# Performance work log

Measured on AMD Instinct MI355X. Metric: run time of the kernel, lower is better.

The kernel has to match this reference:

```python
import jax, jax.numpy as jnp
import numpy as np

H_DIM = 64; GRID = 8; G = GRID * GRID; NEIGH = 2.0
ATT = 1024; EMB = 4
S = 32; P = 64; B = S * P


def setup_inputs() -> dict:
    key = jax.random.key(0)
    ks = jax.random.split(key, 20)
    bounds = jnp.arange(0, B + 1, P, dtype=jnp.int32)
    seq_start_end = jnp.stack([bounds[:-1], bounds[1:]], axis=1)  # (S,2) uniform scenes
    def lin(k, fan_in, shape):
        return jax.random.normal(k, shape, jnp.float32) / np.sqrt(fan_in)
    return {
        "h_states": jax.random.normal(ks[0], (1, B, H_DIM), jnp.float32),
        "seq_start_end": seq_start_end,
        "end_pos": jax.random.uniform(ks[1], (B, 2), jnp.float32) * 4.0,
        "rel_pos": jax.random.normal(ks[2], (B, 2), jnp.float32),
        # Attention_Decoder params
        "W_enc": lin(ks[3], H_DIM, (H_DIM, ATT)), "b_enc": jnp.zeros((ATT,), jnp.float32),
        "W_dec": lin(ks[4], H_DIM, (H_DIM, ATT)), "b_dec": jnp.zeros((ATT,), jnp.float32),
        "w_full": lin(ks[5], ATT, (ATT,)), "b_full": jnp.zeros((), jnp.float32),
        "W_embed": lin(ks[6], 4, (4, EMB)), "b_embed": jnp.zeros((EMB,), jnp.float32),
        "W_out": lin(ks[7], H_DIM + EMB, (H_DIM + EMB, ATT)), "b_out": jnp.zeros((ATT,), jnp.float32),
        # mlp_pool params (Linear -> BatchNorm -> ReLU)
        "W_mlp": lin(ks[8], ATT, (ATT, ATT)), "b_mlp": jnp.zeros((ATT,), jnp.float32),
        "bn_gamma": jnp.ones((ATT,), jnp.float32), "bn_beta": jnp.zeros((ATT,), jnp.float32),
    }


def social_pool(h, end_pos):
    # h: (B, H), end_pos: (B, 2); uniform scenes S x P
    pos = end_pos.reshape(S, P, 2)
    hid = h.reshape(S, P, H_DIM)
    ax = pos[:, :, None, 0]; ay = pos[:, :, None, 1]  # anchor (S,P,1)
    ox = pos[:, None, :, 0]; oy = pos[:, None, :, 1]  # other  (S,1,P)
    half = NEIGH / 2
    tl_x = ax - half; tl_y = ay + half
    br_x = ax + half; br_y = ay - half
    cell_x = jnp.floor((ox - tl_x) / NEIGH * GRID)
    cell_y = jnp.floor((tl_y - oy) / NEIGH * GRID)
    grid = (cell_x + cell_y * GRID).astype(jnp.int32)  # (S,P,P)
    oob = (ox >= br_x) | (ox <= tl_x) | (oy >= tl_y) | (oy <= br_y)
    oob = oob | jnp.eye(P, dtype=bool)[None]  # self-pairs excluded (within_bound[0::P+1]=1)
    anchor_off = (jnp.arange(P, dtype=jnp.int32) * G)[None, :, None]
    idx = jnp.where(oob, 0, grid + 1 + anchor_off)  # slot 0 = dump slot
    seq_off = (jnp.arange(S, dtype=jnp.int32) * (P * G + 1))[:, None, None]
    flat_idx = (idx + seq_off).reshape(-1)
    vals = jnp.broadcast_to(hid[:, None, :, :], (S, P, P, H_DIM)).reshape(-1, H_DIM)
    buf = jnp.zeros((S * (P * G + 1), H_DIM), h.dtype).at[flat_idx].add(vals)
    buf = buf.reshape(S, P * G + 1, H_DIM)[:, 1:, :]  # drop dump slot per scene
    return buf.reshape(B, G, H_DIM)


def reference(h_states, seq_start_end, end_pos, rel_pos,
              W_enc, b_enc, W_dec, b_dec, w_full, b_full,
              W_embed, b_embed, W_out, b_out, W_mlp, b_mlp, bn_gamma, bn_beta):
    del seq_start_end  # uniform scene layout baked into S, P
    h = h_states.reshape(-1, H_DIM)                      # (B, H)
    enc = social_pool(h, end_pos)                        # (B, G, H)
    dec_a = h @ W_dec + b_dec                            # (B, ATT)
    enc_a = jnp.einsum('bgh,ha->bga', enc, W_enc) + b_enc
    scores = jax.nn.relu(enc_a + dec_a[:, None, :]) @ w_full + b_full  # (B, G)
    alpha = jax.nn.softmax(scores, axis=-1)
    ctx = jnp.einsum('bg,bgh->bh', alpha, enc)           # (B, H)
    embed_info = jnp.concatenate([end_pos, rel_pos], axis=1)  # (B, 4)
    emb = jax.nn.relu(embed_info @ W_embed + b_embed)
    out = jax.nn.relu(jnp.concatenate([ctx, emb], axis=1) @ W_out + b_out)  # (B, ATT)
    # mlp_pool: Linear -> BatchNorm1d (training-mode batch stats) -> ReLU
    x = out @ W_mlp + b_mlp
    mu = jnp.mean(x, axis=0)
    var = jnp.var(x, axis=0)
    x = (x - mu) * jax.lax.rsqrt(var + 1e-5) * bn_gamma + bn_beta
    return jax.nn.relu(x)
```

## Files before the change

kernel.cpp:

```cpp
#include <hip/hip_runtime.h>
#include <hip/hip_bf16.h>
#include <math.h>

#define H_DIM 64
#define G 64
#define ATT 1024
#define EMB 4
#define P 64
#define BB 2048
#define MAXROWS 129088
#define PREP_BLOCKS 817
#define MAGICF 0x13579BDF

typedef __attribute__((ext_vector_type(8))) short short8;
typedef __attribute__((ext_vector_type(4))) float floatx4;

__device__ inline ushort f2bf(float v) {
    __hip_bfloat16 b = __float2bfloat16(v);
    return *(ushort*)&b;
}
__device__ inline float bf2f(ushort u) {
    union { float f; unsigned u32; } x;
    x.u32 = ((unsigned)u) << 16;
    return x.f;
}

__global__ __launch_bounds__(256) void prep_kernel(const float* __restrict__ h,
                                                   const float* __restrict__ end_pos,
                                                   const float* __restrict__ W_enc,
                                                   const float* __restrict__ W_dec,
                                                   const float* __restrict__ W_out,
                                                   const float* __restrict__ W_mlp,
                                                   ushort* __restrict__ enc,
                                                   ushort* __restrict__ h_bf,
                                                   ushort* __restrict__ Wte,
                                                   ushort* __restrict__ Wdt,
                                                   ushort* __restrict__ Wot,
                                                   ushort* __restrict__ Wt,
                                                   int* __restrict__ rowidx,
                                                   int* __restrict__ cntA,
                                                   int* __restrict__ baseA,
                                                   int* __restrict__ counter,
                                                   float* __restrict__ sums,
                                                   int* __restrict__ flag) {
    __shared__ float tileT[64][65];
    __shared__ int nzS[4], baseSh[4];

    int blk = blockIdx.x;
    int t = threadIdx.x;

    if (blk == 0) {
        if (t < 64) __hip_atomic_store(&counter[t], 0, __ATOMIC_RELAXED, __HIP_MEMORY_SCOPE_AGENT);
        int* sz = (int*)sums;
        for (int i = t; i < 2048; i += 256)
            __hip_atomic_store(&sz[i], 0, __ATOMIC_RELAXED, __HIP_MEMORY_SCOPE_AGENT);
        __syncthreads();
        if (t == 0) __hip_atomic_store(flag, MAGICF, __ATOMIC_RELEASE, __HIP_MEMORY_SCOPE_AGENT);
    } else if (blk <= 512) {
        int wv = t >> 6, lane = t & 63;
        int b = (blk - 1) * 4 + wv;
        int s = b >> 6, i = b & 63;
        const float* pseq = end_pos + (size_t)s * P * 2;
        const float* hrow = h + (size_t)s * P * H_DIM;

        float2 pj = ((const float2*)pseq)[lane];
        float ax = __shfl(pj.x, i), ay = __shfl(pj.y, i);
        float tlx = ax - 1.f, tly = ay + 1.f, brx = ax + 1.f, bry = ay - 1.f;
        bool oob = (pj.x >= brx) || (pj.x <= tlx) || (pj.y >= tly) || (pj.y <= bry) || (lane == i);
        int cx = (int)floorf((pj.x - tlx) * 4.0f);
        int cy = (int)floorf((tly - pj.y) * 4.0f);
        int g = cx + cy * 8;

        unsigned long long hitmask = __ballot(!oob);
        unsigned long long m = hitmask, cellmask = 0ull;
        while (m) {
            int j = __builtin_ctzll(m); m &= m - 1;
            int gj = __shfl(g, j);
            cellmask |= 1ull << gj;
        }
        int n_nz = __popcll(cellmask);
        if (lane == 0) nzS[wv] = n_nz;

        h_bf[(size_t)b * 64 + lane] = f2bf(h[(size_t)b * 64 + lane]);

        __syncthreads();
        if (t == 0) {
            while (__hip_atomic_load(flag, __ATOMIC_ACQUIRE, __HIP_MEMORY_SCOPE_AGENT) != MAGICF) {}
            int n0 = nzS[0], n1 = nzS[1], n2 = nzS[2], n3 = nzS[3];
            int base = atomicAdd(counter, n0 + n1 + n2 + n3);
            baseSh[0] = base;
            baseSh[1] = base + n0;
            baseSh[2] = base + n0 + n1;
            baseSh[3] = base + n0 + n1 + n2;
        }
        __syncthreads();
        int base = baseSh[wv];
        if (lane == 0) { cntA[b] = n_nz; baseA[b] = base; }

        unsigned long long cm = cellmask;
        int slot = 0;
        while (cm) {
            int gg = __builtin_ctzll(cm); cm &= cm - 1;
            unsigned long long jm = __ballot((!oob) && (g == gg));
            float sum = 0.f;
            while (jm) {
                int j = __builtin_ctzll(jm); jm &= jm - 1;
                sum += hrow[j * H_DIM + lane];
            }
            enc[((size_t)(b * G + gg)) * H_DIM + lane] = f2bf(sum);
            if (lane == 0) rowidx[base + slot] = b * G + gg;
            ++slot;
        }
    } else if (blk <= 528) {
        int n0 = (blk - 513) * 64;
        #pragma unroll
        for (int idx = 0; idx < 16; ++idx) {
            int flat = t + 256 * idx;
            int k = flat >> 6, c = flat & 63;
            tileT[k][c] = W_enc[(size_t)k * ATT + n0 + c];
        }
        __syncthreads();
        #pragma unroll
        for (int idx = 0; idx < 16; ++idx) {
            int flat = t + 256 * idx;
            int n = flat >> 6, k = flat & 63;
            Wte[(size_t)(n0 + n) * 64 + k] = f2bf(tileT[k][n]);
        }
    } else if (blk <= 544) {
        int n0 = (blk - 529) * 64;
        #pragma unroll
        for (int idx = 0; idx < 16; ++idx) {
            int flat = t + 256 * idx;
            int k = flat >> 6, c = flat & 63;
            tileT[k][c] = W_dec[(size_t)k * ATT + n0 + c];
        }
        __syncthreads();
        #pragma unroll
        for (int idx = 0; idx < 16; ++idx) {
            int flat = t + 256 * idx;
            int n = flat >> 6, k = flat & 63;
            Wdt[(size_t)(n0 + n) * 64 + k] = f2bf(tileT[k][n]);
        }
    } else if (blk <= 560) {
        int n0 = (blk - 545) * 64;
        int n = t & 63, kg = t >> 6;
        #pragma unroll
        for (int kk = 0; kk < 24; ++kk) {
            int k = kg * 24 + kk;
            float v = (k < 68) ? W_out[(size_t)k * ATT + n0 + n] : 0.f;
            Wot[(size_t)(n0 + n) * 96 + k] = f2bf(v);
        }
    } else {
        int idx2 = blk - 561;
        int k0 = (idx2 & 15) * 64, n0 = (idx2 >> 4) * 64;
        #pragma unroll
        for (int idx = 0; idx < 16; ++idx) {
            int flat = t + 256 * idx;
            int r = flat >> 6, c = flat & 63;
            tileT[r][c] = W_mlp[(size_t)(k0 + r) * ATT + n0 + c];
        }
        __syncthreads();
        #pragma unroll
        for (int idx = 0; idx < 16; ++idx) {
            int flat = t + 256 * idx;
            int r = flat >> 6, c = flat & 63;
            Wt[(size_t)(n0 + r) * ATT + k0 + c] = f2bf(tileT[c][r]);
        }
    }
}

__global__ __launch_bounds__(256) void dec_mfma_kernel(const ushort* __restrict__ A,
                                                       const ushort* __restrict__ Bt,
                                                       const float* __restrict__ b_dec,
                                                       const float* __restrict__ b_enc,
                                                       const float* __restrict__ w_full,
                                                       float* __restrict__ dec_r,
                                                       float* __restrict__ s_part) {
    int t = threadIdx.x;
    int w = t >> 6, lane = t & 63;
    int lm = lane & 15, q = lane >> 4;
    int m0 = blockIdx.x * 64, n1 = blockIdx.y * 128;
    __shared__ __align__(16) ushort Asm[64][72];
    __shared__ __align__(16) ushort Bsm[128][72];

    #pragma unroll
    for (int i = 0; i < 4; ++i) {
        int flat = t + 256 * i;
        int r = flat >> 4, c4 = (flat & 15) * 4;
        *(uint2*)&Asm[r][c4] = *(const uint2*)&A[(size_t)(m0 + r) * 64 + c4];
    }
    #pragma unroll
    for (int i = 0; i < 8; ++i) {
        int flat = t + 256 * i;
        int r = flat >> 4, c4 = (flat & 15) * 4;
        *(uint2*)&Bsm[r][c4] = *(const uint2*)&Bt[(size_t)(n1 + r) * 64 + c4];
    }
    __syncthreads();

    floatx4 acc[4][2];
    #pragma unroll
    for (int mt = 0; mt < 4; ++mt)
        #pragma unroll
        for (int nt = 0; nt < 2; ++nt) acc[mt][nt] = (floatx4){0.f, 0.f, 0.f, 0.f};

    #pragma unroll
    for (int ks = 0; ks < 64; ks += 32) {
        short8 af[4], bfr[2];
        #pragma unroll
        for (int mt = 0; mt < 4; ++mt)
            af[mt] = *(const short8*)&Asm[mt * 16 + lm][ks + q * 8];
        #pragma unroll
        for (int nt = 0; nt < 2; ++nt)
            bfr[nt] = *(const short8*)&Bsm[w * 32 + nt * 16 + lm][ks + q * 8];
        #pragma unroll
        for (int mt = 0; mt < 4; ++mt)
            #pragma unroll
            for (int nt = 0; nt < 2; ++nt)
                acc[mt][nt] = __builtin_amdgcn_mfma_f32_16x16x32_bf16(af[mt], bfr[nt], acc[mt][nt], 0, 0, 0);
    }

    float part[4][4];
    #pragma unroll
    for (int mt = 0; mt < 4; ++mt)
        #pragma unroll
        for (int r = 0; r < 4; ++r) part[mt][r] = 0.f;

    #pragma unroll
    for (int nt = 0; nt < 2; ++nt) {
        int col = n1 + w * 32 + nt * 16 + lm;
        float bcol = b_dec[col] + b_enc[col];
        float wf = w_full[col];
        #pragma unroll
        for (int mt = 0; mt < 4; ++mt)
            #pragma unroll
            for (int r = 0; r < 4; ++r) {
                int row = m0 + mt * 16 + q * 4 + r;
                float v = acc[mt][nt][r] + bcol;
                dec_r[(size_t)row * ATT + col] = v;
                part[mt][r] += fmaxf(v, 0.f) * wf;
            }
    }
    #pragma unroll
    for (int mt = 0; mt < 4; ++mt)
        #pragma unroll
        for (int r = 0; r < 4; ++r) {
            float v = part[mt][r];
            v += __shfl_xor(v, 1); v += __shfl_xor(v, 2);
            v += __shfl_xor(v, 4); v += __shfl_xor(v, 8);
            part[mt][r] = v;
        }
    if (lm == 0) {
        int sp = blockIdx.y * 4 + w;
        #pragma unroll
        for (int mt = 0; mt < 4; ++mt)
            #pragma unroll
            for (int r = 0; r < 4; ++r)
                s_part[(size_t)sp * 2048 + m0 + mt * 16 + q * 4 + r] = part[mt][r];
    }
}

__global__ __launch_bounds__(256) void scoresC_mfma_kernel(const ushort* __restrict__ enc,
                                                           const int* __restrict__ rowidx,
                                                           const int* __restrict__ counter,
                                                           const float* __restrict__ dec_r,
                                                           const ushort* __restrict__ Wte,
                                                           const float* __restrict__ w_full,
                                                           const float* __restrict__ b_full,
                                                           float* __restrict__ score_c) {
    int M = counter[0];
    int row0 = blockIdx.x * 64;
    if (row0 >= M) return;
    int t = threadIdx.x;
    int w = t >> 6, lane = t & 63;
    int lm = lane & 15, q = lane >> 4;

    __shared__ __align__(16) ushort AS[64][72];
    __shared__ __align__(16) ushort BS[256][72];
    __shared__ int rowS[64];
    __shared__ float redS[4][64];

    if (t < 64) rowS[t] = (row0 + t < M) ? rowidx[row0 + t] : 0;
    __syncthreads();
    #pragma unroll
    for (int i = 0; i < 4; ++i) {
        int flat = t + 256 * i;
        int r = flat >> 4, c4 = (flat & 15) * 4;
        *(uint2*)&AS[r][c4] = *(const uint2*)&enc[(size_t)rowS[r] * 64 + c4];
    }
    int bbr[16];
    #pragma unroll
    for (int mt = 0; mt < 4; ++mt)
        #pragma unroll
        for (int r = 0; r < 4; ++r)
            bbr[mt * 4 + r] = rowS[mt * 16 + q * 4 + r] >> 6;

    float part[4][4];
    #pragma unroll
    for (int mt = 0; mt < 4; ++mt)
        #pragma unroll
        for (int r = 0; r < 4; ++r) part[mt][r] = 0.f;

    for (int c = 0; c < 4; ++c) {
        __syncthreads();
        #pragma unroll
        for (int i = 0; i < 16; ++i) {
            int flat = t + 256 * i;
            int r = flat >> 4, c4 = (flat & 15) * 4;
            *(uint2*)&BS[r][c4] = *(const uint2*)&Wte[(size_t)(c * 256 + r) * 64 + c4];
        }
        __syncthreads();

        floatx4 acc[4][4];
        #pragma unroll
        for (int mt = 0; mt < 4; ++mt)
            #pragma unroll
            for (int nt = 0; nt < 4; ++nt) acc[mt][nt] = (floatx4){0.f, 0.f, 0.f, 0.f};

        #pragma unroll
        for (int ks = 0; ks < 64; ks += 32) {
            short8 af[4], bfr[4];
            #pragma unroll
            for (int mt = 0; mt < 4; ++mt)
                af[mt] = *(const short8*)&AS[mt * 16 + lm][ks + q * 8];
            #pragma unroll
            for (int nt = 0; nt < 4; ++nt)
                bfr[nt] = *(const short8*)&BS[w * 64 + nt * 16 + lm][ks + q * 8];
            #pragma unroll
            for (int mt = 0; mt < 4; ++mt)
                #pragma unroll
                for (int nt = 0; nt < 4; ++nt)
                    acc[mt][nt] = __builtin_amdgcn_mfma_f32_16x16x32_bf16(af[mt], bfr[nt], acc[mt][nt], 0, 0, 0);
        }

        int colbase = c * 256 + w * 64;
        #pragma unroll
        for (int nt = 0; nt < 4; ++nt) {
            int col = colbase + nt * 16 + lm;
            float wf = w_full[col];
            #pragma unroll
            for (int mt = 0; mt < 4; ++mt)
                #pragma unroll
                for (int r = 0; r < 4; ++r) {
                    float v = acc[mt][nt][r] + dec_r[(size_t)bbr[mt * 4 + r] * ATT + col];
                    part[mt][r] += fmaxf(v, 0.f) * wf;
                }
        }
    }
    #pragma unroll
    for (int mt = 0; mt < 4; ++mt)
        #pragma unroll
        for (int r = 0; r < 4; ++r) {
            float v = part[mt][r];
            v += __shfl_xor(v, 1); v += __shfl_xor(v, 2);
            v += __shfl_xor(v, 4); v += __shfl_xor(v, 8);
            part[mt][r] = v;
        }
    if (lm == 0) {
        #pragma unroll
        for (int mt = 0; mt < 4; ++mt)
            #pragma unroll
            for (int r = 0; r < 4; ++r)
                redS[w][mt * 16 + q * 4 + r] = part[mt][r];
    }
    __syncthreads();
    if (t < 64) {
        int row = row0 + t;
        if (row < M)
            score_c[row] = redS[0][t] + redS[1][t] + redS[2][t] + redS[3][t] + b_full[0];
    }
}

__global__ __launch_bounds__(64) void softmax_ctx_kernel(const float* __restrict__ score_c,
                                                         const int* __restrict__ rowidx,
                                                         const int* __restrict__ cntA,
                                                         const int* __restrict__ baseA,
                                                         const float* __restrict__ s_part,
                                                         const ushort* __restrict__ enc,
                                                         const float* __restrict__ end_pos,
                                                         const float* __restrict__ rel_pos,
                                                         const float* __restrict__ W_embed,
                                                         const float* __restrict__ b_embed,
                                                         const float* __restrict__ b_full,
                                                         ushort* __restrict__ ctx_bf) {
    int b = blockIdx.x, t = threadIdx.x;
    int cnt = cntA[b], base = baseA[b];
    float sp = (t < 32) ? s_part[(size_t)t * 2048 + b] : 0.f;
    #pragma unroll
    for (int o = 32; o > 0; o >>= 1) sp += __shfl_xor(sp, o);
    float se = sp + b_full[0];
    float sc = se;
    int ri = 0;
    if (t < cnt) { sc = score_c[base + t]; ri = rowidx[base + t]; }
    float mx = sc;
    #pragma unroll
    for (int o = 32; o > 0; o >>= 1) mx = fmaxf(mx, __shfl_xor(mx, o));
    float e = expf(sc - mx);
    float ssum = e;
    #pragma unroll
    for (int o = 32; o > 0; o >>= 1) ssum += __shfl_xor(ssum, o);
    __shared__ float aS[G];
    __shared__ int rS[G];
    aS[t] = e / ssum;
    rS[t] = ri;
    __syncthreads();
    float ctx = 0.f;
    for (int i = 0; i < cnt; ++i)
        ctx += aS[i] * bf2f(enc[(size_t)rS[i] * H_DIM + t]);
    ctx_bf[(size_t)b * 96 + t] = f2bf(ctx);
    if (t < EMB) {
        float e0 = end_pos[2*b], e1 = end_pos[2*b+1], e2 = rel_pos[2*b], e3 = rel_pos[2*b+1];
        float v = b_embed[t] + e0 * W_embed[0*EMB + t] + e1 * W_embed[1*EMB + t]
                             + e2 * W_embed[2*EMB + t] + e3 * W_embed[3*EMB + t];
        ctx_bf[(size_t)b * 96 + 64 + t] = f2bf(v > 0.f ? v : 0.f);
    }
    if (t < 28) ctx_bf[(size_t)b * 96 + 68 + t] = 0;
}

__global__ __launch_bounds__(256) void out_mfma_kernel(const ushort* __restrict__ A,
                                                       const ushort* __restrict__ Bt,
                                                       const float* __restrict__ bias,
                                                       ushort* __restrict__ out) {
    int t = threadIdx.x;
    int w = t >> 6, lane = t & 63;
    int lm = lane & 15, q = lane >> 4;
    int m0 = blockIdx.x * 64, n1 = blockIdx.y * 128;
    __shared__ __align__(16) ushort Asm[64][104];
    __shared__ __align__(16) ushort Bsm[128][104];

    {
        int r = t >> 2, pp = t & 3;
        #pragma unroll
        for (int ii = 0; ii < 3; ++ii) {
            int c8 = (pp * 3 + ii) * 8;
            *(uint4*)&Asm[r][c8] = *(const uint4*)&A[(size_t)(m0 + r) * 96 + c8];
        }
    }
    {
        int r = t >> 1, pp = t & 1;
        #pragma unroll
        for (int ii = 0; ii < 6; ++ii) {
            int c8 = (pp * 6 + ii) * 8;
            *(uint4*)&Bsm[r][c8] = *(const uint4*)&Bt[(size_t)(n1 + r) * 96 + c8];
        }
    }
    __syncthreads();

    floatx4 acc[4][2];
    #pragma unroll
    for (int mt = 0; mt < 4; ++mt)
        #pragma unroll
        for (int nt = 0; nt < 2; ++nt) acc[mt][nt] = (floatx4){0.f, 0.f, 0.f, 0.f};

    #pragma unroll
    for (int ks = 0; ks < 96; ks += 32) {
        short8 af[4], bfr[2];
        #pragma unroll
        for (int mt = 0; mt < 4; ++mt)
            af[mt] = *(const short8*)&Asm[mt * 16 + lm][ks + q * 8];
        #pragma unroll
        for (int nt = 0; nt < 2; ++nt)
            bfr[nt] = *(const short8*)&Bsm[w * 32 + nt * 16 + lm][ks + q * 8];
        #pragma unroll
        for (int mt = 0; mt < 4; ++mt)
            #pragma unroll
            for (int nt = 0; nt < 2; ++nt)
                acc[mt][nt] = __builtin_amdgcn_mfma_f32_16x16x32_bf16(af[mt], bfr[nt], acc[mt][nt], 0, 0, 0);
    }
    #pragma unroll
    for (int nt = 0; nt < 2; ++nt) {
        int col = n1 + w * 32 + nt * 16 + lm;
        float bv = bias[col];
        #pragma unroll
        for (int mt = 0; mt < 4; ++mt)
            #pragma unroll
            for (int r = 0; r < 4; ++r) {
                int row = m0 + mt * 16 + q * 4 + r;
                out[(size_t)row * ATT + col] = f2bf(fmaxf(acc[mt][nt][r] + bv, 0.f));
            }
    }
}

__global__ __launch_bounds__(256) void mlp_mfma_kernel(const ushort* __restrict__ A,
                                                       const ushort* __restrict__ Bt,
                                                       const float* __restrict__ bias,
                                                       float* __restrict__ X,
                                                       float* __restrict__ sums) {
    int t = threadIdx.x;
    int w = t >> 6, lane = t & 63;
    int lm = lane & 15, q = lane >> 4;
    int m0 = blockIdx.x * 64, n0 = blockIdx.y * 64;
    __shared__ __align__(16) ushort Asm[64][72];
    __shared__ __align__(16) ushort Bsm[64][72];

    floatx4 acc[4];
    #pragma unroll
    for (int mt = 0; mt < 4; ++mt) acc[mt] = (floatx4){0.f, 0.f, 0.f, 0.f};

    for (int k0 = 0; k0 < 1024; k0 += 64) {
        __syncthreads();
        #pragma unroll
        for (int i = 0; i < 4; ++i) {
            int flat = t + 256 * i;
            int r = flat >> 4, c4 = (flat & 15) * 4;
            *(uint2*)&Asm[r][c4] = *(const uint2*)&A[(size_t)(m0 + r) * 1024 + k0 + c4];
            *(uint2*)&Bsm[r][c4] = *(const uint2*)&Bt[(size_t)(n0 + r) * 1024 + k0 + c4];
        }
        __syncthreads();
        #pragma unroll
        for (int ks = 0; ks < 64; ks += 32) {
            short8 af[4], bfr;
            #pragma unroll
            for (int mt = 0; mt < 4; ++mt)
                af[mt] = *(const short8*)&Asm[mt * 16 + lm][ks + q * 8];
            bfr = *(const short8*)&Bsm[w * 16 + lm][ks + q * 8];
            #pragma unroll
            for (int mt = 0; mt < 4; ++mt)
                acc[mt] = __builtin_amdgcn_mfma_f32_16x16x32_bf16(af[mt], bfr, acc[mt], 0, 0, 0);
        }
    }
    int col = n0 + w * 16 + lm;
    float bv = bias[col];
    float s1 = 0.f, s2 = 0.f;
    #pragma unroll
    for (int mt = 0; mt < 4; ++mt)
        #pragma unroll
        for (int r = 0; r < 4; ++r) {
            int row = m0 + mt * 16 + q * 4 + r;
            float v = acc[mt][r] + bv;
            X[(size_t)row * 1024 + col] = v;
            s1 += v; s2 += v * v;
        }
    s1 += __shfl_xor(s1, 16); s1 += __shfl_xor(s1, 32);
    s2 += __shfl_xor(s2, 16); s2 += __shfl_xor(s2, 32);
    if (q == 0) {
        atomicAdd(&sums[col], s1);
        atomicAdd(&sums[ATT + col], s2);
    }
}

__global__ __launch_bounds__(256) void bn_kernel(const float* __restrict__ X,
                                                 const float* __restrict__ sums,
                                                 const float* __restrict__ gamma,
                                                 const float* __restrict__ beta,
                                                 float* __restrict__ out) {
    size_t i4 = ((size_t)blockIdx.x * 256 + threadIdx.x) * 4;
    int f = (int)(i4 & 1023);
    float4 xv = *(const float4*)&X[i4];
    float4 s1 = *(const float4*)&sums[f];
    float4 s2 = *(const float4*)&sums[ATT + f];
    float4 gm = *(const float4*)&gamma[f];
    float4 bt = *(const float4*)&beta[f];
    float4 ov;
    float mu, var, v;
    mu = s1.x * (1.f / BB); var = s2.x * (1.f / BB) - mu * mu;
    v = (xv.x - mu) * rsqrtf(var + 1e-5f) * gm.x + bt.x; ov.x = v > 0.f ? v : 0.f;
    mu = s1.y * (1.f / BB); var = s2.y * (1.f / BB) - mu * mu;
    v = (xv.y - mu) * rsqrtf(var + 1e-5f) * gm.y + bt.y; ov.y = v > 0.f ? v : 0.f;
    mu = s1.z * (1.f / BB); var = s2.z * (1.f / BB) - mu * mu;
    v = (xv.z - mu) * rsqrtf(var + 1e-5f) * gm.z + bt.z; ov.z = v > 0.f ? v : 0.f;
    mu = s1.w * (1.f / BB); var = s2.w * (1.f / BB) - mu * mu;
    v = (xv.w - mu) * rsqrtf(var + 1e-5f) * gm.w + bt.w; ov.w = v > 0.f ? v : 0.f;
    *(float4*)&out[i4] = ov;
}

extern "C" void kernel_launch(void* const* d_in, const int* in_sizes, int n_in,
                              void* d_out, int out_size, void* d_ws, size_t ws_size,
                              hipStream_t stream) {
    const float* h        = (const float*)d_in[0];
    const float* end_pos  = (const float*)d_in[2];
    const float* rel_pos  = (const float*)d_in[3];
    const float* W_enc    = (const float*)d_in[4];
    const float* b_enc    = (const float*)d_in[5];
    const float* W_dec    = (const float*)d_in[6];
    const float* b_dec    = (const float*)d_in[7];
    const float* w_full   = (const float*)d_in[8];
    const float* b_full   = (const float*)d_in[9];
    const float* W_embed  = (const float*)d_in[10];
    const float* b_embed  = (const float*)d_in[11];
    const float* W_out    = (const float*)d_in[12];
    const float* b_out    = (const float*)d_in[13];
    const float* W_mlp    = (const float*)d_in[14];
    const float* b_mlp    = (const float*)d_in[15];
    const float* bn_gamma = (const float*)d_in[16];
    const float* bn_beta  = (const float*)d_in[17];

    float* ws = (float*)d_ws;
    ushort* enc     = (ushort*)ws;
    ushort* h_bf    = (ushort*)(ws + 4194304);
    ushort* Wte     = (ushort*)(ws + 4259840);
    ushort* Wdt     = (ushort*)(ws + 4292608);
    ushort* Wot     = (ushort*)(ws + 4325376);
    ushort* Wt      = (ushort*)(ws + 4374528);
    ushort* ctx_bf  = (ushort*)(ws + 4898816);
    ushort* out_bf  = (ushort*)(ws + 4997120);
    float*  x       = ws + 6045696;
    float*  dec_r   = ws + 8388608;
    int*    rowidx  = (int*)(ws + 10485760);
    float*  score_c = ws + 10616832;
    int*    cntA    = (int*)(ws + 10747904);
    int*    baseA   = (int*)(ws + 10749952);
    int*    counter = (int*)(ws + 10752000);
    float*  sums    = ws + 10752064;
    float*  s_part  = ws + 10754112;
    int*    flag    = (int*)(ws + 10819648);

    prep_kernel<<<PREP_BLOCKS, 256, 0, stream>>>(h, end_pos, W_enc, W_dec, W_out, W_mlp,
                                                 enc, h_bf, Wte, Wdt, Wot, Wt,
                                                 rowidx, cntA, baseA, counter, sums, flag);
    dec_mfma_kernel<<<dim3(32, 8), 256, 0, stream>>>(h_bf, Wdt, b_dec, b_enc, w_full, dec_r, s_part);
    scoresC_mfma_kernel<<<MAXROWS / 64, 256, 0, stream>>>(enc, rowidx, counter, dec_r, Wte,
                                                          w_full, b_full, score_c);
    softmax_ctx_kernel<<<BB, 64, 0, stream>>>(score_c, rowidx, cntA, baseA, s_part, enc,
                                              end_pos, rel_pos, W_embed, b_embed, b_full, ctx_bf);
    out_mfma_kernel<<<dim3(32, 8), 256, 0, stream>>>(ctx_bf, Wot, b_out, out_bf);
    mlp_mfma_kernel<<<dim3(32, 16), 256, 0, stream>>>(out_bf, Wt, b_mlp, x, sums);
    bn_kernel<<<2048, 256, 0, stream>>>(x, sums, bn_gamma, bn_beta, (float*)d_out);
}
```

Before: 167.2 us.

## Fuse decoder GEMM into prep kernel, converting h and W_dec on the fly

The decoder projection GEMM (h @ W_dec plus bias, relu dot with w_full) now runs as extra blocks inside the prep kernel. Those blocks read fp32 h and W_dec directly and convert them to bf16 in shared memory. This removes one kernel launch and the intermediate h_bf and Wdt buffers, along with their global round-trip. The cost is a larger shared-memory footprint per prep block, which may reduce occupancy for the other block roles, and uncoalesced transposing loads of W_dec.

```diff
diff --git a/kernel.cpp b/kernel.cpp
--- a/kernel.cpp
+++ b/kernel.cpp
@@ -9,7 +9,7 @@
 #define P 64
 #define BB 2048
 #define MAXROWS 129088
-#define PREP_BLOCKS 817
+#define K1_BLOCKS 1057
 #define MAGICF 0x13579BDF
 
 typedef __attribute__((ext_vector_type(8))) short short8;
@@ -31,19 +31,22 @@
                                                    const float* __restrict__ W_dec,
                                                    const float* __restrict__ W_out,
                                                    const float* __restrict__ W_mlp,
+                                                   const float* __restrict__ b_dec,
+                                                   const float* __restrict__ b_enc,
+                                                   const float* __restrict__ w_full,
                                                    ushort* __restrict__ enc,
-                                                   ushort* __restrict__ h_bf,
                                                    ushort* __restrict__ Wte,
-                                                   ushort* __restrict__ Wdt,
                                                    ushort* __restrict__ Wot,
                                                    ushort* __restrict__ Wt,
+                                                   float* __restrict__ dec_r,
+                                                   float* __restrict__ s_part,
                                                    int* __restrict__ rowidx,
                                                    int* __restrict__ cntA,
                                                    int* __restrict__ baseA,
                                                    int* __restrict__ counter,
                                                    float* __restrict__ sums,
                                                    int* __restrict__ flag) {
-    __shared__ float tileT[64][65];
+    __shared__ __align__(16) char sm1[28672];
     __shared__ int nzS[4], baseSh[4];
 
     int blk = blockIdx.x;
@@ -56,9 +59,91 @@
             __hip_atomic_store(&sz[i], 0, __ATOMIC_RELAXED, __HIP_MEMORY_SCOPE_AGENT);
         __syncthreads();
         if (t == 0) __hip_atomic_store(flag, MAGICF, __ATOMIC_RELEASE, __HIP_MEMORY_SCOPE_AGENT);
-    } else if (blk <= 512) {
+    } else if (blk <= 256) {
+        int idx = blk - 1;
+        int m0 = (idx & 31) * 64, n1 = (idx >> 5) * 128;
+        int w = t >> 6, lane = t & 63;
+        int lm = lane & 15, q = lane >> 4;
+        ushort (*Asm)[72] = (ushort(*)[72])sm1;
+        ushort (*Bsm)[72] = (ushort(*)[72])(sm1 + 9216);
+
+        #pragma unroll
+        for (int i = 0; i < 16; ++i) {
+            int flat = t + 256 * i;
+            int r = flat >> 6, k = flat & 63;
+            Asm[r][k] = f2bf(h[(size_t)(m0 + r) * 64 + k]);
+        }
+        #pragma unroll
+        for (int i = 0; i < 32; ++i) {
+            int flat = t + 256 * i;
+            int k = flat >> 7, n = flat & 127;
+            Bsm[n][k] = f2bf(W_dec[(size_t)k * ATT + n1 + n]);
+        }
+        __syncthreads();
+
+        floatx4 acc[4][2];
+        #pragma unroll
+        for (int mt = 0; mt < 4; ++mt)
+            #pragma unroll
+            for (int nt = 0; nt < 2; ++nt) acc[mt][nt] = (floatx4){0.f, 0.f, 0.f, 0.f};
+
+        #pragma unroll
+        for (int ks = 0; ks < 64; ks += 32) {
+            short8 af[4], bfr[2];
+            #pragma unroll
+            for (int mt = 0; mt < 4; ++mt)
+                af[mt] = *(const short8*)&Asm[mt * 16 + lm][ks + q * 8];
+            #pragma unroll
+            for (int nt = 0; nt < 2; ++nt)
+                bfr[nt] = *(const short8*)&Bsm[w * 32 + nt * 16 + lm][ks + q * 8];
+            #pragma unroll
+            for (int mt = 0; mt < 4; ++mt)
+                #pragma unroll
+                for (int nt = 0; nt < 2; ++nt)
+                    acc[mt][nt] = __builtin_amdgcn_mfma_f32_16x16x32_bf16(af[mt], bfr[nt], acc[mt][nt], 0, 0, 0);
+        }
+
+        float part[4][4];
+        #pragma unroll
+        for (int mt = 0; mt < 4; ++mt)
+            #pragma unroll
+            for (int r = 0; r < 4; ++r) part[mt][r] = 0.f;
+
+        #pragma unroll
+        for (int nt = 0; nt < 2; ++nt) {
+            int col = n1 + w * 32 + nt * 16 + lm;
+            float bcol = b_dec[col] + b_enc[col];
+            float wf = w_full[col];
+            #pragma unroll
+            for (int mt = 0; mt < 4; ++mt)
+                #pragma unroll
+                for (int r = 0; r < 4; ++r) {
+                    int row = m0 + mt * 16 + q * 4 + r;
+                    float v = acc[mt][nt][r] + bcol;
+                    dec_r[(size_t)row * ATT + col] = v;
+                    part[mt][r] += fmaxf(v, 0.f) * wf;
+                }
+        }
+        #pragma unroll
+        for (int mt = 0; mt < 4; ++mt)
+            #pragma unroll
+            for (int r = 0; r < 4; ++r) {
+                float v = part[mt][r];
+                v += __shfl_xor(v, 1); v += __shfl_xor(v, 2);
+                v += __shfl_xor(v, 4); v += __shfl_xor(v, 8);
+                part[mt][r] = v;
+            }
+        if (lm == 0) {
+            int sp = (idx >> 5) * 4 + w;
+            #pragma unroll
+            for (int mt = 0; mt < 4; ++mt)
+                #pragma unroll
+                for (int r = 0; r < 4; ++r)
+                    s_part[(size_t)sp * 2048 + m0 + mt * 16 + q * 4 + r] = part[mt][r];
+        }
+    } else if (blk <= 768) {
         int wv = t >> 6, lane = t & 63;
-        int b = (blk - 1) * 4 + wv;
+        int b = (blk - 257) * 4 + wv;
         int s = b >> 6, i = b & 63;
         const float* pseq = end_pos + (size_t)s * P * 2;
         const float* hrow = h + (size_t)s * P * H_DIM;
@@ -80,8 +165,6 @@
         }
         int n_nz = __popcll(cellmask);
         if (lane == 0) nzS[wv] = n_nz;
-
-        h_bf[(size_t)b * 64 + lane] = f2bf(h[(size_t)b * 64 + lane]);
 
         __syncthreads();
         if (t == 0) {
@@ -111,8 +194,9 @@
             if (lane == 0) rowidx[base + slot] = b * G + gg;
             ++slot;
         }
-    } else if (blk <= 528) {
-        int n0 = (blk - 513) * 64;
+    } else if (blk <= 784) {
+        float (*tileT)[65] = (float(*)[65])sm1;
+        int n0 = (blk - 769) * 64;
         #pragma unroll
         for (int idx = 0; idx < 16; ++idx) {
             int flat = t + 256 * idx;
@@ -126,23 +210,8 @@
             int n = flat >> 6, k = flat & 63;
             Wte[(size_t)(n0 + n) * 64 + k] = f2bf(tileT[k][n]);
         }
-    } else if (blk <= 544) {
-        int n0 = (blk - 529) * 64;
-        #pragma unroll
-        for (int idx = 0; idx < 16; ++idx) {
-            int flat = t + 256 * idx;
-            int k = flat >> 6, c = flat & 63;
-            tileT[k][c] = W_dec[(size_t)k * ATT + n0 + c];
-        }
-        __syncthreads();
-        #pragma unroll
-        for (int idx = 0; idx < 16; ++idx) {
-            int flat = t + 256 * idx;
-            int n = flat >> 6, k = flat & 63;
-            Wdt[(size_t)(n0 + n) * 64 + k] = f2bf(tileT[k][n]);
-        }
-    } else if (blk <= 560) {
-        int n0 = (blk - 545) * 64;
+    } else if (blk <= 800) {
+        int n0 = (blk - 785) * 64;
         int n = t & 63, kg = t >> 6;
         #pragma unroll
         for (int kk = 0; kk < 24; ++kk) {
@@ -151,7 +220,8 @@
             Wot[(size_t)(n0 + n) * 96 + k] = f2bf(v);
         }
     } else {
-        int idx2 = blk - 561;
+        float (*tileT)[65] = (float(*)[65])sm1;
+        int idx2 = blk - 801;
         int k0 = (idx2 & 15) * 64, n0 = (idx2 >> 4) * 64;
         #pragma unroll
         for (int idx = 0; idx < 16; ++idx) {
@@ -166,96 +236,6 @@
             int r = flat >> 6, c = flat & 63;
             Wt[(size_t)(n0 + r) * ATT + k0 + c] = f2bf(tileT[c][r]);
         }
-    }
-}
-
-__global__ __launch_bounds__(256) void dec_mfma_kernel(const ushort* __restrict__ A,
-                                                       const ushort* __restrict__ Bt,
-                                                       const float* __restrict__ b_dec,
-                                                       const float* __restrict__ b_enc,
-                                                       const float* __restrict__ w_full,
-                                                       float* __restrict__ dec_r,
-                                                       float* __restrict__ s_part) {
-    int t = threadIdx.x;
-    int w = t >> 6, lane = t & 63;
-    int lm = lane & 15, q = lane >> 4;
-    int m0 = blockIdx.x * 64, n1 = blockIdx.y * 128;
-    __shared__ __align__(16) ushort Asm[64][72];
-    __shared__ __align__(16) ushort Bsm[128][72];
-
-    #pragma unroll
-    for (int i = 0; i < 4; ++i) {
-        int flat = t + 256 * i;
-        int r = flat >> 4, c4 = (flat & 15) * 4;
-        *(uint2*)&Asm[r][c4] = *(const uint2*)&A[(size_t)(m0 + r) * 64 + c4];
-    }
-    #pragma unroll
-    for (int i = 0; i < 8; ++i) {
-        int flat = t + 256 * i;
-        int r = flat >> 4, c4 = (flat & 15) * 4;
-        *(uint2*)&Bsm[r][c4] = *(const uint2*)&Bt[(size_t)(n1 + r) * 64 + c4];
-    }
-    __syncthreads();
-
-    floatx4 acc[4][2];
-    #pragma unroll
-    for (int mt = 0; mt < 4; ++mt)
-        #pragma unroll
-        for (int nt = 0; nt < 2; ++nt) acc[mt][nt] = (floatx4){0.f, 0.f, 0.f, 0.f};
-
-    #pragma unroll
-    for (int ks = 0; ks < 64; ks += 32) {
-        short8 af[4], bfr[2];
-        #pragma unroll
-        for (int mt = 0; mt < 4; ++mt)
-            af[mt] = *(const short8*)&Asm[mt * 16 + lm][ks + q * 8];
-        #pragma unroll
-        for (int nt = 0; nt < 2; ++nt)
-            bfr[nt] = *(const short8*)&Bsm[w * 32 + nt * 16 + lm][ks + q * 8];
-        #pragma unroll
-        for (int mt = 0; mt < 4; ++mt)
-            #pragma unroll
-            for (int nt = 0; nt < 2; ++nt)
-                acc[mt][nt] = __builtin_amdgcn_mfma_f32_16x16x32_bf16(af[mt], bfr[nt], acc[mt][nt], 0, 0, 0);
-    }
-
-    float part[4][4];
-    #pragma unroll
-    for (int mt = 0; mt < 4; ++mt)
-        #pragma unroll
-        for (int r = 0; r < 4; ++r) part[mt][r] = 0.f;
-
-    #pragma unroll
-    for (int nt = 0; nt < 2; ++nt) {
-        int col = n1 + w * 32 + nt * 16 + lm;
-        float bcol = b_dec[col] + b_enc[col];
-        float wf = w_full[col];
-        #pragma unroll
-        for (int mt = 0; mt < 4; ++mt)
-            #pragma unroll
-            for (int r = 0; r < 4; ++r) {
-                int row = m0 + mt * 16 + q * 4 + r;
-                float v = acc[mt][nt][r] + bcol;
-                dec_r[(size_t)row * ATT + col] = v;
-                part[mt][r] += fmaxf(v, 0.f) * wf;
-            }
-    }
-    #pragma unroll
-    for (int mt = 0; mt < 4; ++mt)
-        #pragma unroll
-        for (int r = 0; r < 4; ++r) {
-            float v = part[mt][r];
-            v += __shfl_xor(v, 1); v += __shfl_xor(v, 2);
-            v += __shfl_xor(v, 4); v += __shfl_xor(v, 8);
-            part[mt][r] = v;
-        }
-    if (lm == 0) {
-        int sp = blockIdx.y * 4 + w;
-        #pragma unroll
-        for (int mt = 0; mt < 4; ++mt)
-            #pragma unroll
-            for (int r = 0; r < 4; ++r)
-                s_part[(size_t)sp * 2048 + m0 + mt * 16 + q * 4 + r] = part[mt][r];
     }
 }
 
@@ -586,9 +566,7 @@
 
     float* ws = (float*)d_ws;
     ushort* enc     = (ushort*)ws;
-    ushort* h_bf    = (ushort*)(ws + 4194304);
     ushort* Wte     = (ushort*)(ws + 4259840);
-    ushort* Wdt     = (ushort*)(ws + 4292608);
     ushort* Wot     = (ushort*)(ws + 4325376);
     ushort* Wt      = (ushort*)(ws + 4374528);
     ushort* ctx_bf  = (ushort*)(ws + 4898816);
@@ -604,10 +582,10 @@
     float*  s_part  = ws + 10754112;
     int*    flag    = (int*)(ws + 10819648);
 
-    prep_kernel<<<PREP_BLOCKS, 256, 0, stream>>>(h, end_pos, W_enc, W_dec, W_out, W_mlp,
-                                                 enc, h_bf, Wte, Wdt, Wot, Wt,
-                                                 rowidx, cntA, baseA, counter, sums, flag);
-    dec_mfma_kernel<<<dim3(32, 8), 256, 0, stream>>>(h_bf, Wdt, b_dec, b_enc, w_full, dec_r, s_part);
+    prep_kernel<<<K1_BLOCKS, 256, 0, stream>>>(h, end_pos, W_enc, W_dec, W_out, W_mlp,
+                                               b_dec, b_enc, w_full,
+                                               enc, Wte, Wot, Wt, dec_r, s_part,
+                                               rowidx, cntA, baseA, counter, sums, flag);
     scoresC_mfma_kernel<<<MAXROWS / 64, 256, 0, stream>>>(enc, rowidx, counter, dec_r, Wte,
                                                           w_full, b_full, score_c);
     softmax_ctx_kernel<<<BB, 64, 0, stream>>>(score_c, rowidx, cntA, baseA, s_part, enc,
```

Measured after the change: 163.6 us. 2.1% less time.
